# Kernel tuning notes

Hardware: AMD Instinct MI355X
Metric: run time of the kernel (lower is better)

The kernel has to match this reference:

```python
import jax, jax.numpy as jnp
import numpy as np

N_NODES = 50000
N_EDGES = 800000
N_GRAPHS = 64
IN_CH = 128
HID_CH = 128
FC_CH = 128


def setup_inputs() -> dict:
    key = jax.random.key(0)
    ks = jax.random.split(key, 12)

    def lin_w(k, fan_in, fan_out):
        return jax.random.normal(k, (fan_in, fan_out), jnp.float32) * (1.0 / np.sqrt(fan_in))

    return {
        "x": jax.random.normal(ks[0], (N_NODES, IN_CH), jnp.float32),
        "edge_index": jax.random.randint(ks[1], (2, N_EDGES), 0, N_NODES, dtype=jnp.int64),
        "batch_vec": jnp.sort(jax.random.randint(ks[2], (N_NODES,), 0, N_GRAPHS, dtype=jnp.int64)),
        "W1": lin_w(ks[3], IN_CH, HID_CH),
        "b1": jnp.zeros((HID_CH,), jnp.float32),
        "W2": lin_w(ks[4], HID_CH, HID_CH),
        "b2": jnp.zeros((HID_CH,), jnp.float32),
        "W3": lin_w(ks[5], HID_CH, FC_CH),
        "b3": jnp.zeros((FC_CH,), jnp.float32),
        "fcW1": lin_w(ks[6], FC_CH, IN_CH),
        "fcb1": jnp.zeros((IN_CH,), jnp.float32),
        "fcW2": lin_w(ks[7], IN_CH, 2),
        "fcb2": jnp.zeros((2,), jnp.float32),
    }


def reference(x, edge_index, batch_vec, W1, b1, W2, b2, W3, b3, fcW1, fcb1, fcW2, fcb2):
    n = x.shape[0]
    row, col = edge_index[0], edge_index[1]  # src -> dst

    # GCN symmetric normalization with self-loops: deg[j] = in-degree(j) + 1
    deg = jnp.zeros((n,), x.dtype).at[col].add(1.0) + 1.0
    inv_sqrt = jax.lax.rsqrt(deg)
    edge_norm = inv_sqrt[row] * inv_sqrt[col]  # [E]
    self_norm = (inv_sqrt * inv_sqrt)[:, None]  # [N,1], self-loop weight 1/deg

    def gcn(h, W, b):
        h = h @ W  # [N, out]
        agg = jnp.zeros_like(h).at[col].add(h[row] * edge_norm[:, None])
        return agg + h * self_norm + b

    h = jax.nn.relu(gcn(x, W1, b1))
    h = jax.nn.relu(gcn(h, W2, b2))
    h = jax.nn.relu(gcn(h, W3, b3))
    h = jax.nn.relu(h @ fcW1 + fcb1)
    h = h @ fcW2 + fcb2  # [N, 2]

    # global mean pool per graph
    sums = jax.ops.segment_sum(h, batch_vec, num_segments=N_GRAPHS)
    cnts = jax.ops.segment_sum(jnp.ones((n,), h.dtype), batch_vec, num_segments=N_GRAPHS)
    pooled = sums / jnp.maximum(cnts, 1.0)[:, None]  # [G, 2]
    return jax.nn.softmax(pooled, axis=1)
```

## Files before the change

### kernel.cpp

```cpp
#include <hip/hip_runtime.h>


#define CH 128
#define BSH 7
#define SEG 4096
#define EPW 4096
#define SA 40
#define SAF 136
#define SC 132
#define SC8 144

typedef unsigned short ushortT;
typedef unsigned int uintT;
typedef unsigned char ucharT;
typedef __attribute__((ext_vector_type(8))) short short8;
typedef __attribute__((ext_vector_type(4))) float floatx4;
typedef __attribute__((ext_vector_type(2))) float floatx2;

__device__ __forceinline__ float bf2f(uintT u) {
    return __uint_as_float(u << 16);
}
__device__ __forceinline__ ushortT f2bf(float f) {
    uintT x = __float_as_uint(f);
    return (ushortT)((x + 0x7fffu + ((x >> 16) & 1u)) >> 16);
}
__device__ __forceinline__ void dec4(uintT u, float* o) {
    floatx2 lo = __builtin_amdgcn_cvt_pk_f32_fp8((int)u, false);
    floatx2 hi = __builtin_amdgcn_cvt_pk_f32_fp8((int)u, true);
    o[0] = lo.x; o[1] = lo.y; o[2] = hi.x; o[3] = hi.y;
}

__global__ void k_zero(int* __restrict__ bfill, int NB, float* __restrict__ acc, int nacc) {
    int t = threadIdx.x;
    for (int i = t; i < NB; i += 256) bfill[i] = 0;
    for (int i = t; i < nacc; i += 256) acc[i] = 0.f;
}

__global__ __launch_bounds__(256) void k_bin(const int* __restrict__ row,
                                             const int* __restrict__ col,
                                             int* __restrict__ bfill,
                                             uintT* __restrict__ seg,
                                             int E, int NB) {
    __shared__ uintT staged[EPW];
    __shared__ int target[EPW];
    __shared__ int sval[512];
    __shared__ int horig[512];
    __shared__ int pcnt[512];
    __shared__ int gbase[512];
    const int t = threadIdx.x;
    const int e0 = blockIdx.x * EPW;
    const int cnt = min(EPW, E - e0);

    sval[t] = 0; sval[t + 256] = 0;
    __syncthreads();

    int er[16], ec[16];
#pragma unroll
    for (int i = 0; i < 16; ++i) {
        int le = i * 256 + t;
        if (le < cnt) {
            er[i] = row[e0 + le];
            ec[i] = col[e0 + le];
            atomicAdd(&sval[ec[i] >> BSH], 1);
        }
    }
    __syncthreads();
    horig[t] = sval[t]; horig[t + 256] = sval[t + 256];
    __syncthreads();
    for (int off = 1; off < 512; off <<= 1) {
        int a = (t >= off) ? sval[t - off] : 0;
        int b2 = sval[t + 256 - off];
        __syncthreads();
        sval[t] += a;
        sval[t + 256] += b2;
        __syncthreads();
    }
    for (int b = t; b < 512; b += 256) {
        int h = horig[b];
        pcnt[b] = sval[b] - h;
        gbase[b] = (h > 0 && b < NB) ? atomicAdd(&bfill[b], h) : 0;
    }
    __syncthreads();
#pragma unroll
    for (int i = 0; i < 16; ++i) {
        int le = i * 256 + t;
        if (le < cnt) {
            int b = ec[i] >> BSH;
            int j = atomicAdd(&pcnt[b], 1);
            staged[j] = (uintT)er[i] | ((uintT)ec[i] << 16);
            int lo = sval[b] - horig[b];
            target[j] = b * SEG + gbase[b] + (j - lo);
        }
    }
    __syncthreads();
    for (int s = t; s < cnt; s += 256) seg[target[s]] = staged[s];
}

__global__ __launch_bounds__(512) void k_binvs_bscan(const int* __restrict__ bfill,
                                                     const uintT* __restrict__ seg,
                                                     float* __restrict__ invs,
                                                     int* __restrict__ bbase,
                                                     int* __restrict__ indptr,
                                                     int NB, int N, int E) {
    const int b = blockIdx.x;
    const int t = threadIdx.x;
    if (b < NB) {
        __shared__ int h[128];
        if (t < 128) h[t] = 0;
        __syncthreads();
        int cnt = bfill[b];
        const uintT* sp = seg + (size_t)b * SEG;
        for (int s = t; s < cnt; s += 512) atomicAdd(&h[(sp[s] >> 16) & 127], 1);
        __syncthreads();
        int d = b * 128 + t;
        if (t < 128 && d < N) invs[d] = rsqrtf((float)h[t] + 1.0f);
    } else {
        __shared__ int s[512];
        int v = (t < NB) ? bfill[t] : 0;
        s[t] = v;
        __syncthreads();
        for (int off = 1; off < 512; off <<= 1) {
            int a = (t >= off) ? s[t - off] : 0;
            __syncthreads();
            s[t] += a;
            __syncthreads();
        }
        if (t < NB) bbase[t] = s[t] - v;
        if (t == 0) indptr[N] = E;
    }
}

__global__ __launch_bounds__(256) void k_scatterprep(const int* __restrict__ bfill,
                                                     const int* __restrict__ bbase,
                                                     const uintT* __restrict__ seg,
                                                     const float* __restrict__ invs,
                                                     int* __restrict__ indptr,
                                                     uintT* __restrict__ epack,
                                                     const float* __restrict__ X,
                                                     ucharT* __restrict__ Xb,
                                                     const float* __restrict__ w0,
                                                     const float* __restrict__ w1,
                                                     const float* __restrict__ w2,
                                                     const float* __restrict__ w3,
                                                     ushortT* __restrict__ Whi,
                                                     int N, int NB, int total4) {
    const int t = threadIdx.x;
    if ((int)blockIdx.x < NB) {
        __shared__ uintT staged[SEG];
        __shared__ int h[128];
        __shared__ int sc[128];
        __shared__ int pc[128];
        const int b = blockIdx.x;
        const int cnt = bfill[b];
        const int base = bbase[b];
        const uintT* sp = seg + (size_t)b * SEG;

        if (t < 128) h[t] = 0;
        __syncthreads();
        for (int s = t; s < cnt; s += 256) atomicAdd(&h[(sp[s] >> 16) & 127], 1);
        __syncthreads();
        if (t < 128) sc[t] = h[t];
        __syncthreads();
        for (int off = 1; off < 128; off <<= 1) {
            int a = (t >= off && t < 128) ? sc[t - off] : 0;
            __syncthreads();
            if (t < 128) sc[t] += a;
            __syncthreads();
        }
        if (t < 128) {
            int excl = sc[t] - h[t];
            pc[t] = excl;
            int d = b * 128 + t;
            if (d < N) indptr[d] = base + excl;
        }
        __syncthreads();
        for (int s = t; s < cnt; s += 256) {
            uintT rc = sp[s];
            int src = (int)(rc & 0xffffu), dst = (int)(rc >> 16);
            int j = atomicAdd(&pc[dst & 127], 1);
            float nrm = invs[src] * invs[dst];
            staged[j] = (uintT)src | ((uintT)f2bf(nrm) << 16);
        }
        __syncthreads();
        for (int s = t; s < cnt; s += 256) epack[base + s] = staged[s];
    } else if ((int)blockIdx.x < NB + 256) {
        int idx = (blockIdx.x - NB) * 256 + t;
        int m = idx >> 14;
        int r = idx & 16383;
        int n = r >> 7;
        int k = r & 127;
        const float* W = (m == 0) ? w0 : (m == 1) ? w1 : (m == 2) ? w2 : w3;
        Whi[m * 16384 + n * CH + k] = f2bf(W[k * CH + n]);
    } else {
        int i = (blockIdx.x - NB - 256) * 256 + t;
        if (i < total4) {
            float4 v = reinterpret_cast<const float4*>(X)[i];
            int r0 = __builtin_amdgcn_cvt_pk_fp8_f32(v.x, v.y, 0, false);
            int r1 = __builtin_amdgcn_cvt_pk_fp8_f32(v.z, v.w, r0, true);
            reinterpret_cast<int*>(Xb)[i] = r1;
        }
    }
}

__global__ __launch_bounds__(256) void k_agg(const ucharT* __restrict__ H8,
                                             const uintT* __restrict__ epack,
                                             const int* __restrict__ indptr,
                                             const float* __restrict__ invs,
                                             ucharT* __restrict__ Z8, int N) {
    const int wave = threadIdx.x >> 6, lane = threadIdx.x & 63;
    const int sub = lane >> 4;
    const int l = lane & 15;
    const int node = blockIdx.x * 16 + wave * 4 + sub;
    if (node >= N) return;

    const uint2* H2 = reinterpret_cast<const uint2*>(H8);

    float acc[8];
    {
        float sn = invs[node];
        float sn2 = sn * sn;
        uint2 h = H2[(size_t)node * 16 + l];
        float d[8];
        dec4(h.x, d); dec4(h.y, d + 4);
#pragma unroll
        for (int j = 0; j < 8; ++j) acc[j] = sn2 * d[j];
    }

    int p = indptr[node];
    int p1 = indptr[node + 1];
    for (; p + 8 <= p1; p += 8) {
        uintT e[8];
#pragma unroll
        for (int i = 0; i < 8; ++i) e[i] = epack[p + i];
        uint2 g[8];
#pragma unroll
        for (int i = 0; i < 8; ++i) g[i] = H2[(size_t)(int)(e[i] & 0xffffu) * 16 + l];
#pragma unroll
        for (int i = 0; i < 8; ++i) {
            float wv = bf2f(e[i] >> 16);
            float d[8];
            dec4(g[i].x, d); dec4(g[i].y, d + 4);
#pragma unroll
            for (int j = 0; j < 8; ++j) acc[j] += wv * d[j];
        }
    }
    if (p + 4 <= p1) {
        uintT e[4];
#pragma unroll
        for (int i = 0; i < 4; ++i) e[i] = epack[p + i];
        uint2 g[4];
#pragma unroll
        for (int i = 0; i < 4; ++i) g[i] = H2[(size_t)(int)(e[i] & 0xffffu) * 16 + l];
#pragma unroll
        for (int i = 0; i < 4; ++i) {
            float wv = bf2f(e[i] >> 16);
            float d[8];
            dec4(g[i].x, d); dec4(g[i].y, d + 4);
#pragma unroll
            for (int j = 0; j < 8; ++j) acc[j] += wv * d[j];
        }
        p += 4;
    }
    for (; p < p1; ++p) {
        uintT e = epack[p];
        uint2 g = H2[(size_t)(int)(e & 0xffffu) * 16 + l];
        float wv = bf2f(e >> 16);
        float d[8];
        dec4(g.x, d); dec4(g.y, d + 4);
#pragma unroll
        for (int j = 0; j < 8; ++j) acc[j] += wv * d[j];
    }

    uint2 o;
    {
        int r0 = __builtin_amdgcn_cvt_pk_fp8_f32(acc[0], acc[1], 0, false);
        r0 = __builtin_amdgcn_cvt_pk_fp8_f32(acc[2], acc[3], r0, true);
        int r1 = __builtin_amdgcn_cvt_pk_fp8_f32(acc[4], acc[5], 0, false);
        r1 = __builtin_amdgcn_cvt_pk_fp8_f32(acc[6], acc[7], r1, true);
        o.x = (uintT)r0; o.y = (uintT)r1;
    }
    reinterpret_cast<uint2*>(Z8)[(size_t)node * 16 + l] = o;
}

__global__ __launch_bounds__(256) void k_gemm(const ucharT* __restrict__ In8,
                                              const ushortT* __restrict__ Whi,
                                              const float* __restrict__ Bias,
                                              ucharT* __restrict__ Out8, int N) {
    __shared__ ushortT smem[128 * SC];
    ushortT* As = smem;
    ushortT* Ws = smem + 128 * SA;
    ushortT* Cs = smem;

    const int tid = threadIdx.x;
    const int wave = tid >> 6, lane = tid & 63;
    const int quad = lane >> 4, l15 = lane & 15;
    const int mBase = (wave >> 1) * 64, nBase = (wave & 1) * 64;
    const int row0 = blockIdx.x * 128;
    const int r = tid >> 1, half = tid & 1;

    floatx4 acc[4][4];
    const floatx4 zero4 = {0.f, 0.f, 0.f, 0.f};
#pragma unroll
    for (int i = 0; i < 4; i++)
#pragma unroll
        for (int j = 0; j < 4; j++) acc[i][j] = zero4;

    for (int ks = 0; ks < 4; ++ks) {
        {
            int grow = row0 + r;
            uint4 a8 = {0, 0, 0, 0};
            if (grow < N)
                a8 = *reinterpret_cast<const uint4*>(
                    In8 + (size_t)grow * CH + ks * 32 + half * 16);
            uintT wds[4] = {a8.x, a8.y, a8.z, a8.w};
            uintT ob[8];
#pragma unroll
            for (int q = 0; q < 4; ++q) {
                float d[4];
                dec4(wds[q], d);
                ob[2 * q] = (uintT)f2bf(d[0]) | ((uintT)f2bf(d[1]) << 16);
                ob[2 * q + 1] = (uintT)f2bf(d[2]) | ((uintT)f2bf(d[3]) << 16);
            }
            uint4* dd = reinterpret_cast<uint4*>(&As[r * SA + half * 16]);
            dd[0] = uint4{ob[0], ob[1], ob[2], ob[3]};
            dd[1] = uint4{ob[4], ob[5], ob[6], ob[7]};
            const uint4* sh = reinterpret_cast<const uint4*>(Whi + r * CH + ks * 32 + half * 16);
            uint4* dh = reinterpret_cast<uint4*>(&Ws[r * SA + half * 16]);
            dh[0] = sh[0]; dh[1] = sh[1];
        }
        __syncthreads();

        short8 af[4], wf[4];
#pragma unroll
        for (int mt = 0; mt < 4; ++mt)
            af[mt] = *reinterpret_cast<const short8*>(&As[(mBase + mt * 16 + l15) * SA + quad * 8]);
#pragma unroll
        for (int nt = 0; nt < 4; ++nt)
            wf[nt] = *reinterpret_cast<const short8*>(&Ws[(nBase + nt * 16 + l15) * SA + quad * 8]);
#pragma unroll
        for (int mt = 0; mt < 4; ++mt)
#pragma unroll
            for (int nt = 0; nt < 4; ++nt)
                acc[mt][nt] = __builtin_amdgcn_mfma_f32_16x16x32_bf16(af[mt], wf[nt], acc[mt][nt], 0, 0, 0);
        __syncthreads();
    }

    float bb[4];
#pragma unroll
    for (int nt = 0; nt < 4; ++nt) bb[nt] = Bias[nBase + nt * 16 + l15];

    ucharT* Cs8 = reinterpret_cast<ucharT*>(Cs);
#pragma unroll
    for (int mt = 0; mt < 4; ++mt)
#pragma unroll
        for (int nt = 0; nt < 4; ++nt)
#pragma unroll
            for (int r4 = 0; r4 < 4; ++r4) {
                int lrow = mBase + mt * 16 + quad * 4 + r4;
                float v = fmaxf(acc[mt][nt][r4] + bb[nt], 0.f);
                int f8 = __builtin_amdgcn_cvt_pk_fp8_f32(v, 0.f, 0, false);
                Cs8[lrow * SC8 + nBase + nt * 16 + l15] = (ucharT)(f8 & 0xff);
            }
    __syncthreads();
    {
        int grow = row0 + r;
        if (grow < N) {
            const uint4* s4 = reinterpret_cast<const uint4*>(&Cs8[r * SC8 + half * 64]);
            uint4* dst = reinterpret_cast<uint4*>(Out8 + (size_t)grow * CH + half * 64);
#pragma unroll
            for (int q = 0; q < 4; ++q) dst[q] = s4[q];
        }
    }
}

__global__ __launch_bounds__(256) void k_tail(const ucharT* __restrict__ Z8,
                                              const ushortT* __restrict__ W3hi,
                                              const float* __restrict__ B3,
                                              const ushortT* __restrict__ F1hi,
                                              const float* __restrict__ FB1,
                                              const float* __restrict__ FW2,
                                              const float* __restrict__ FB2,
                                              const int* __restrict__ batch,
                                              float* __restrict__ sums,
                                              float* __restrict__ cnts, int N) {
    __shared__ ushortT Hf[128 * SAF];
    __shared__ ushortT Ws[128 * SA];
    __shared__ float rp0[256];
    __shared__ float rp1[256];
    __shared__ float ls[192];

    const int tid = threadIdx.x;
    const int wave = tid >> 6, lane = tid & 63;
    const int quad = lane >> 4, l15 = lane & 15;
    const int mBase = (wave >> 1) * 64, nBase = (wave & 1) * 64;
    const int row0 = blockIdx.x * 128;
    const int r = tid >> 1, half = tid & 1;

    {
        int grow = row0 + r;
        uint4 a8 = {0, 0, 0, 0}, b8 = {0, 0, 0, 0}, c8 = {0, 0, 0, 0}, d8v = {0, 0, 0, 0};
        if (grow < N) {
            const uint4* s = reinterpret_cast<const uint4*>(Z8 + (size_t)grow * CH + half * 64);
            a8 = s[0]; b8 = s[1]; c8 = s[2]; d8v = s[3];
        }
        uintT wds[16] = {a8.x, a8.y, a8.z, a8.w, b8.x, b8.y, b8.z, b8.w,
                         c8.x, c8.y, c8.z, c8.w, d8v.x, d8v.y, d8v.z, d8v.w};
#pragma unroll
        for (int q = 0; q < 16; ++q) {
            float d[4];
            dec4(wds[q], d);
            uint2 o;
            o.x = (uintT)f2bf(d[0]) | ((uintT)f2bf(d[1]) << 16);
            o.y = (uintT)f2bf(d[2]) | ((uintT)f2bf(d[3]) << 16);
            *reinterpret_cast<uint2*>(&Hf[r * SAF + half * 64 + q * 4]) = o;
        }
    }

    floatx4 acc[4][4];
    const floatx4 zero4 = {0.f, 0.f, 0.f, 0.f};
#pragma unroll
    for (int i = 0; i < 4; i++)
#pragma unroll
        for (int j = 0; j < 4; j++) acc[i][j] = zero4;

    for (int ks = 0; ks < 4; ++ks) {
        {
            const uint4* sh = reinterpret_cast<const uint4*>(W3hi + r * CH + ks * 32 + half * 16);
            uint4* dh = reinterpret_cast<uint4*>(&Ws[r * SA + half * 16]);
            dh[0] = sh[0]; dh[1] = sh[1];
        }
        __syncthreads();
        short8 af[4], wf[4];
#pragma unroll
        for (int mt = 0; mt < 4; ++mt)
            af[mt] = *reinterpret_cast<const short8*>(&Hf[(mBase + mt * 16 + l15) * SAF + ks * 32 + quad * 8]);
#pragma unroll
        for (int nt = 0; nt < 4; ++nt)
            wf[nt] = *reinterpret_cast<const short8*>(&Ws[(nBase + nt * 16 + l15) * SA + quad * 8]);
#pragma unroll
        for (int mt = 0; mt < 4; ++mt)
#pragma unroll
            for (int nt = 0; nt < 4; ++nt)
                acc[mt][nt] = __builtin_amdgcn_mfma_f32_16x16x32_bf16(af[mt], wf[nt], acc[mt][nt], 0, 0, 0);
        __syncthreads();
    }

    {
        float bb[4];
#pragma unroll
        for (int nt = 0; nt < 4; ++nt) bb[nt] = B3[nBase + nt * 16 + l15];
#pragma unroll
        for (int mt = 0; mt < 4; ++mt)
#pragma unroll
            for (int nt = 0; nt < 4; ++nt)
#pragma unroll
                for (int r4 = 0; r4 < 4; ++r4) {
                    int lrow = mBase + mt * 16 + quad * 4 + r4;
                    float v = fmaxf(acc[mt][nt][r4] + bb[nt], 0.f);
                    Hf[lrow * SAF + nBase + nt * 16 + l15] = f2bf(v);
                }
    }
    __syncthreads();

#pragma unroll
    for (int i = 0; i < 4; i++)
#pragma unroll
        for (int j = 0; j < 4; j++) acc[i][j] = zero4;
    for (int ks = 0; ks < 4; ++ks) {
        {
            const uint4* sh = reinterpret_cast<const uint4*>(F1hi + r * CH + ks * 32 + half * 16);
            uint4* dh = reinterpret_cast<uint4*>(&Ws[r * SA + half * 16]);
            dh[0] = sh[0]; dh[1] = sh[1];
        }
        __syncthreads();
        short8 af[4], wf[4];
#pragma unroll
        for (int mt = 0; mt < 4; ++mt)
            af[mt] = *reinterpret_cast<const short8*>(&Hf[(mBase + mt * 16 + l15) * SAF + ks * 32 + quad * 8]);
#pragma unroll
        for (int nt = 0; nt < 4; ++nt)
            wf[nt] = *reinterpret_cast<const short8*>(&Ws[(nBase + nt * 16 + l15) * SA + quad * 8]);
#pragma unroll
        for (int mt = 0; mt < 4; ++mt)
#pragma unroll
            for (int nt = 0; nt < 4; ++nt)
                acc[mt][nt] = __builtin_amdgcn_mfma_f32_16x16x32_bf16(af[mt], wf[nt], acc[mt][nt], 0, 0, 0);
        __syncthreads();
    }

    {
        float bb[4];
#pragma unroll
        for (int nt = 0; nt < 4; ++nt) bb[nt] = FB1[nBase + nt * 16 + l15];
        float w20[4], w21[4];
#pragma unroll
        for (int nt = 0; nt < 4; ++nt) {
            float2 wv = *reinterpret_cast<const float2*>(FW2 + 2 * (nBase + nt * 16 + l15));
            w20[nt] = wv.x;
            w21[nt] = wv.y;
        }
#pragma unroll
        for (int mt = 0; mt < 4; ++mt)
#pragma unroll
            for (int r4 = 0; r4 < 4; ++r4) {
                float d0 = 0.f, d1 = 0.f;
#pragma unroll
                for (int nt = 0; nt < 4; ++nt) {
                    float v = fmaxf(acc[mt][nt][r4] + bb[nt], 0.f);
                    d0 += v * w20[nt];
                    d1 += v * w21[nt];
                }
#pragma unroll
                for (int m = 8; m >= 1; m >>= 1) {
                    d0 += __shfl_xor(d0, m, 64);
                    d1 += __shfl_xor(d1, m, 64);
                }
                if (l15 == 0) {
                    int lrow = mBase + mt * 16 + quad * 4 + r4;
                    rp0[lrow * 2 + (wave & 1)] = d0;
                    rp1[lrow * 2 + (wave & 1)] = d1;
                }
            }
    }
    if (tid < 192) ls[tid] = 0.f;
    __syncthreads();

    if (tid < 128) {
        int node = row0 + tid;
        if (node < N) {
            float d0 = rp0[tid * 2] + rp0[tid * 2 + 1] + FB2[0];
            float d1 = rp1[tid * 2] + rp1[tid * 2 + 1] + FB2[1];
            int g = batch[node];
            atomicAdd(&ls[g], d0);
            atomicAdd(&ls[64 + g], d1);
            atomicAdd(&ls[128 + g], 1.0f);
        }
    }
    __syncthreads();
    if (tid < 64) {
        float c = ls[128 + tid];
        if (c != 0.f) {
            atomicAdd(&sums[2 * tid], ls[tid]);
            atomicAdd(&sums[2 * tid + 1], ls[64 + tid]);
            atomicAdd(&cnts[tid], c);
        }
    }
}

__global__ void k_softmax(const float* __restrict__ sums, const float* __restrict__ cnts,
                          float* __restrict__ out, int G) {
    int g = blockIdx.x * blockDim.x + threadIdx.x;
    if (g < G) {
        float c = fmaxf(cnts[g], 1.0f);
        float p0 = sums[2 * g] / c;
        float p1 = sums[2 * g + 1] / c;
        float m = fmaxf(p0, p1);
        float e0 = expf(p0 - m), e1 = expf(p1 - m);
        float inv = 1.f / (e0 + e1);
        out[2 * g] = e0 * inv;
        out[2 * g + 1] = e1 * inv;
    }
}

extern "C" void kernel_launch(void* const* d_in, const int* in_sizes, int n_in,
                              void* d_out, int out_size, void* d_ws, size_t ws_size,
                              hipStream_t stream) {
    const float* X   = (const float*)d_in[0];
    const int* EI    = (const int*)d_in[1];
    const int* BATCH = (const int*)d_in[2];
    const float* W1  = (const float*)d_in[3];
    const float* B1  = (const float*)d_in[4];
    const float* W2  = (const float*)d_in[5];
    const float* B2  = (const float*)d_in[6];
    const float* W3  = (const float*)d_in[7];
    const float* B3  = (const float*)d_in[8];
    const float* FW1 = (const float*)d_in[9];
    const float* FB1 = (const float*)d_in[10];
    const float* FW2 = (const float*)d_in[11];
    const float* FB2 = (const float*)d_in[12];

    const int N = in_sizes[0] / CH;
    const int E = in_sizes[1] / 2;
    const int G = out_size / 2;
    const int* rowp = EI;
    const int* colp = EI + E;
    const int NB = (N + 127) >> BSH;

    char* w = (char*)d_ws;
    auto alloc = [&](size_t bytes) -> char* {
        char* p = w;
        w += (bytes + 255) & ~(size_t)255;
        return p;
    };
    ucharT*  Z8    = (ucharT*)alloc((size_t)N * CH);
    ucharT*  Hb8   = (ucharT*)alloc((size_t)N * CH);
    ucharT*  Xb8   = (ucharT*)alloc((size_t)N * CH);
    ushortT* WhiA  = (ushortT*)alloc((size_t)4 * 16384 * 2);
    float* invs    = (float*)alloc((size_t)N * 4);
    int*   indptr  = (int*)alloc((size_t)(N + 1) * 4);
    uintT* epack   = (uintT*)alloc((size_t)E * 4);
    uintT* seg     = (uintT*)alloc((size_t)NB * SEG * 4);
    int*   bfill   = (int*)alloc((size_t)NB * 4);
    int*   bbase   = (int*)alloc((size_t)NB * 4);
    float* sums    = (float*)alloc((size_t)G * 3 * 4);
    float* cnts    = sums + 2 * G;

    const int nbAgg  = (N + 15) / 16;
    const int nbGemm = (N + 127) / 128;
    const int nbBin  = (E + EPW - 1) / EPW;
    const int total4 = N * CH / 4;
    const int nbSP   = NB + 256 + (total4 + 255) / 256;

    k_zero<<<1, 256, 0, stream>>>(bfill, NB, sums, 3 * G);
    k_bin<<<nbBin, 256, 0, stream>>>(rowp, colp, bfill, seg, E, NB);
    k_binvs_bscan<<<NB + 1, 512, 0, stream>>>(bfill, seg, invs, bbase, indptr, NB, N, E);
    k_scatterprep<<<nbSP, 256, 0, stream>>>(bfill, bbase, seg, invs, indptr, epack,
                                            X, Xb8, W1, W2, W3, FW1, WhiA, N, NB, total4);

    k_agg<<<nbAgg, 256, 0, stream>>>(Xb8, epack, indptr, invs, Z8, N);
    k_gemm<<<nbGemm, 256, 0, stream>>>(Z8, WhiA, B1, Hb8, N);
    k_agg<<<nbAgg, 256, 0, stream>>>(Hb8, epack, indptr, invs, Z8, N);
    k_gemm<<<nbGemm, 256, 0, stream>>>(Z8, WhiA + 16384, B2, Hb8, N);
    k_agg<<<nbAgg, 256, 0, stream>>>(Hb8, epack, indptr, invs, Z8, N);
    k_tail<<<nbGemm, 256, 0, stream>>>(Z8, WhiA + 2 * 16384, B3,
                                       WhiA + 3 * 16384, FB1, FW2, FB2,
                                       BATCH, sums, cnts, N);
    k_softmax<<<1, 64, 0, stream>>>(sums, cnts, (float*)d_out, G);
}
```

Baseline: 211.7 us.

## Split node features into two channel-half planes so gather working set fits cache

```diff
diff --git a/kernel.cpp b/kernel.cpp
--- a/kernel.cpp
+++ b/kernel.cpp
@@ -137,7 +137,8 @@
                                                      int* __restrict__ indptr,
                                                      uintT* __restrict__ epack,
                                                      const float* __restrict__ X,
-                                                     ucharT* __restrict__ Xb,
+                                                     ucharT* __restrict__ Xlo,
+                                                     ucharT* __restrict__ Xhi,
                                                      const float* __restrict__ w0,
                                                      const float* __restrict__ w1,
                                                      const float* __restrict__ w2,
@@ -197,29 +198,39 @@
             float4 v = reinterpret_cast<const float4*>(X)[i];
             int r0 = __builtin_amdgcn_cvt_pk_fp8_f32(v.x, v.y, 0, false);
             int r1 = __builtin_amdgcn_cvt_pk_fp8_f32(v.z, v.w, r0, true);
-            reinterpret_cast<int*>(Xb)[i] = r1;
-        }
-    }
-}
-
-__global__ __launch_bounds__(256) void k_agg(const ucharT* __restrict__ H8,
+            int node = i >> 5;
+            int g = i & 31;
+            int* dst = (g < 16) ? reinterpret_cast<int*>(Xlo + (size_t)node * 64) + g
+                                : reinterpret_cast<int*>(Xhi + (size_t)node * 64) + (g - 16);
+            *dst = r1;
+        }
+    }
+}
+
+__global__ __launch_bounds__(256) void k_agg(const ucharT* __restrict__ Hlo,
+                                             const ucharT* __restrict__ Hhi,
                                              const uintT* __restrict__ epack,
                                              const int* __restrict__ indptr,
                                              const float* __restrict__ invs,
-                                             ucharT* __restrict__ Z8, int N) {
+                                             ucharT* __restrict__ Zlo,
+                                             ucharT* __restrict__ Zhi,
+                                             int N, int nbHalf) {
+    const int half = (blockIdx.x >> 2) & 1;
+    const int nb = (blockIdx.x >> 3) * 4 + (blockIdx.x & 3);
+    if (nb >= nbHalf) return;
     const int wave = threadIdx.x >> 6, lane = threadIdx.x & 63;
-    const int sub = lane >> 4;
-    const int l = lane & 15;
-    const int node = blockIdx.x * 16 + wave * 4 + sub;
+    const int ng = lane >> 3;
+    const int l = lane & 7;
+    const int node = nb * 32 + wave * 8 + ng;
     if (node >= N) return;
 
-    const uint2* H2 = reinterpret_cast<const uint2*>(H8);
+    const uint2* H2 = reinterpret_cast<const uint2*>(half ? Hhi : Hlo);
 
     float acc[8];
     {
         float sn = invs[node];
         float sn2 = sn * sn;
-        uint2 h = H2[(size_t)node * 16 + l];
+        uint2 h = H2[(size_t)node * 8 + l];
         float d[8];
         dec4(h.x, d); dec4(h.y, d + 4);
 #pragma unroll
@@ -234,7 +245,7 @@
         for (int i = 0; i < 8; ++i) e[i] = epack[p + i];
         uint2 g[8];
 #pragma unroll
-        for (int i = 0; i < 8; ++i) g[i] = H2[(size_t)(int)(e[i] & 0xffffu) * 16 + l];
+        for (int i = 0; i < 8; ++i) g[i] = H2[(size_t)(int)(e[i] & 0xffffu) * 8 + l];
 #pragma unroll
         for (int i = 0; i < 8; ++i) {
             float wv = bf2f(e[i] >> 16);
@@ -250,7 +261,7 @@
         for (int i = 0; i < 4; ++i) e[i] = epack[p + i];
         uint2 g[4];
 #pragma unroll
-        for (int i = 0; i < 4; ++i) g[i] = H2[(size_t)(int)(e[i] & 0xffffu) * 16 + l];
+        for (int i = 0; i < 4; ++i) g[i] = H2[(size_t)(int)(e[i] & 0xffffu) * 8 + l];
 #pragma unroll
         for (int i = 0; i < 4; ++i) {
             float wv = bf2f(e[i] >> 16);
@@ -263,7 +274,7 @@
     }
     for (; p < p1; ++p) {
         uintT e = epack[p];
-        uint2 g = H2[(size_t)(int)(e & 0xffffu) * 16 + l];
+        uint2 g = H2[(size_t)(int)(e & 0xffffu) * 8 + l];
         float wv = bf2f(e >> 16);
         float d[8];
         dec4(g.x, d); dec4(g.y, d + 4);
@@ -279,13 +290,15 @@
         r1 = __builtin_amdgcn_cvt_pk_fp8_f32(acc[6], acc[7], r1, true);
         o.x = (uintT)r0; o.y = (uintT)r1;
     }
-    reinterpret_cast<uint2*>(Z8)[(size_t)node * 16 + l] = o;
-}
-
-__global__ __launch_bounds__(256) void k_gemm(const ucharT* __restrict__ In8,
+    reinterpret_cast<uint2*>(half ? Zhi : Zlo)[(size_t)node * 8 + l] = o;
+}
+
+__global__ __launch_bounds__(256) void k_gemm(const ucharT* __restrict__ Inlo,
+                                              const ucharT* __restrict__ Inhi,
                                               const ushortT* __restrict__ Whi,
                                               const float* __restrict__ Bias,
-                                              ucharT* __restrict__ Out8, int N) {
+                                              ucharT* __restrict__ Outlo,
+                                              ucharT* __restrict__ Outhi, int N) {
     __shared__ ushortT smem[128 * SC];
     ushortT* As = smem;
     ushortT* Ws = smem + 128 * SA;
@@ -308,10 +321,11 @@
     for (int ks = 0; ks < 4; ++ks) {
         {
             int grow = row0 + r;
+            const ucharT* sbase = (ks < 2) ? Inlo : Inhi;
             uint4 a8 = {0, 0, 0, 0};
             if (grow < N)
                 a8 = *reinterpret_cast<const uint4*>(
-                    In8 + (size_t)grow * CH + ks * 32 + half * 16);
+                    sbase + (size_t)grow * 64 + (ks & 1) * 32 + half * 16);
             uintT wds[4] = {a8.x, a8.y, a8.z, a8.w};
             uintT ob[8];
 #pragma unroll
@@ -366,14 +380,16 @@
         int grow = row0 + r;
         if (grow < N) {
             const uint4* s4 = reinterpret_cast<const uint4*>(&Cs8[r * SC8 + half * 64]);
-            uint4* dst = reinterpret_cast<uint4*>(Out8 + (size_t)grow * CH + half * 64);
+            ucharT* obase = half ? Outhi : Outlo;
+            uint4* dst = reinterpret_cast<uint4*>(obase + (size_t)grow * 64);
 #pragma unroll
             for (int q = 0; q < 4; ++q) dst[q] = s4[q];
         }
     }
 }
 
-__global__ __launch_bounds__(256) void k_tail(const ucharT* __restrict__ Z8,
+__global__ __launch_bounds__(256) void k_tail(const ucharT* __restrict__ Zlo,
+                                              const ucharT* __restrict__ Zhi,
                                               const ushortT* __restrict__ W3hi,
                                               const float* __restrict__ B3,
                                               const ushortT* __restrict__ F1hi,
@@ -398,9 +414,10 @@
 
     {
         int grow = row0 + r;
+        const ucharT* zsrc = half ? Zhi : Zlo;
         uint4 a8 = {0, 0, 0, 0}, b8 = {0, 0, 0, 0}, c8 = {0, 0, 0, 0}, d8v = {0, 0, 0, 0};
         if (grow < N) {
-            const uint4* s = reinterpret_cast<const uint4*>(Z8 + (size_t)grow * CH + half * 64);
+            const uint4* s = reinterpret_cast<const uint4*>(zsrc + (size_t)grow * 64);
             a8 = s[0]; b8 = s[1]; c8 = s[2]; d8v = s[3];
         }
         uintT wds[16] = {a8.x, a8.y, a8.z, a8.w, b8.x, b8.y, b8.z, b8.w,
@@ -592,9 +609,12 @@
         w += (bytes + 255) & ~(size_t)255;
         return p;
     };
-    ucharT*  Z8    = (ucharT*)alloc((size_t)N * CH);
-    ucharT*  Hb8   = (ucharT*)alloc((size_t)N * CH);
-    ucharT*  Xb8   = (ucharT*)alloc((size_t)N * CH);
+    ucharT*  Zlo   = (ucharT*)alloc((size_t)N * 64);
+    ucharT*  Zhi   = (ucharT*)alloc((size_t)N * 64);
+    ucharT*  Hlo   = (ucharT*)alloc((size_t)N * 64);
+    ucharT*  Hhi   = (ucharT*)alloc((size_t)N * 64);
+    ucharT*  Xlo   = (ucharT*)alloc((size_t)N * 64);
+    ucharT*  Xhi   = (ucharT*)alloc((size_t)N * 64);
     ushortT* WhiA  = (ushortT*)alloc((size_t)4 * 16384 * 2);
     float* invs    = (float*)alloc((size_t)N * 4);
     int*   indptr  = (int*)alloc((size_t)(N + 1) * 4);
@@ -605,7 +625,8 @@
     float* sums    = (float*)alloc((size_t)G * 3 * 4);
     float* cnts    = sums + 2 * G;
 
-    const int nbAgg  = (N + 15) / 16;
+    const int nbHalf = (N + 31) / 32;
+    const int nbAgg  = ((nbHalf + 3) / 4) * 8;
     const int nbGemm = (N + 127) / 128;
     const int nbBin  = (E + EPW - 1) / EPW;
     const int total4 = N * CH / 4;
@@ -615,14 +636,15 @@
     k_bin<<<nbBin, 256, 0, stream>>>(rowp, colp, bfill, seg, E, NB);
     k_binvs_bscan<<<NB + 1, 512, 0, stream>>>(bfill, seg, invs, bbase, indptr, NB, N, E);
     k_scatterprep<<<nbSP, 256, 0, stream>>>(bfill, bbase, seg, invs, indptr, epack,
-                                            X, Xb8, W1, W2, W3, FW1, WhiA, N, NB, total4);
-
-    k_agg<<<nbAgg, 256, 0, stream>>>(Xb8, epack, indptr, invs, Z8, N);
-    k_gemm<<<nbGemm, 256, 0, stream>>>(Z8, WhiA, B1, Hb8, N);
-    k_agg<<<nbAgg, 256, 0, stream>>>(Hb8, epack, indptr, invs, Z8, N);
-    k_gemm<<<nbGemm, 256, 0, stream>>>(Z8, WhiA + 16384, B2, Hb8, N);
-    k_agg<<<nbAgg, 256, 0, stream>>>(Hb8, epack, indptr, invs, Z8, N);
-    k_tail<<<nbGemm, 256, 0, stream>>>(Z8, WhiA + 2 * 16384, B3,
+                                            X, Xlo, Xhi, W1, W2, W3, FW1, WhiA,
+                                            N, NB, total4);
+
+    k_agg<<<nbAgg, 256, 0, stream>>>(Xlo, Xhi, epack, indptr, invs, Zlo, Zhi, N, nbHalf);
+    k_gemm<<<nbGemm, 256, 0, stream>>>(Zlo, Zhi, WhiA, B1, Hlo, Hhi, N);
+    k_agg<<<nbAgg, 256, 0, stream>>>(Hlo, Hhi, epack, indptr, invs, Zlo, Zhi, N, nbHalf);
+    k_gemm<<<nbGemm, 256, 0, stream>>>(Zlo, Zhi, WhiA + 16384, B2, Hlo, Hhi, N);
+    k_agg<<<nbAgg, 256, 0, stream>>>(Hlo, Hhi, epack, indptr, invs, Zlo, Zhi, N, nbHalf);
+    k_tail<<<nbGemm, 256, 0, stream>>>(Zlo, Zhi, WhiA + 2 * 16384, B3,
                                        WhiA + 3 * 16384, FB1, FW2, FB2,
                                        BATCH, sums, cnts, N);
     k_softmax<<<1, 64, 0, stream>>>(sums, cnts, (float*)d_out, G);
```

Measured after the change: 210.2 us. No clear change (-0.7%).

## Widen aggregation gathers to 16-byte loads with pipelined edge prefetch

Applied to the files above, without the earlier changes.

```diff
diff --git a/kernel.cpp b/kernel.cpp
--- a/kernel.cpp
+++ b/kernel.cpp
@@ -29,11 +29,8 @@
     floatx2 hi = __builtin_amdgcn_cvt_pk_f32_fp8((int)u, true);
     o[0] = lo.x; o[1] = lo.y; o[2] = hi.x; o[3] = hi.y;
 }
-
-__global__ void k_zero(int* __restrict__ bfill, int NB, float* __restrict__ acc, int nacc) {
-    int t = threadIdx.x;
-    for (int i = t; i < NB; i += 256) bfill[i] = 0;
-    for (int i = t; i < nacc; i += 256) acc[i] = 0.f;
+__device__ __forceinline__ void dec16(uint4 v, float* o) {
+    dec4(v.x, o); dec4(v.y, o + 4); dec4(v.z, o + 8); dec4(v.w, o + 12);
 }
 
 __global__ __launch_bounds__(256) void k_bin(const int* __restrict__ row,
@@ -101,7 +98,9 @@
                                                      float* __restrict__ invs,
                                                      int* __restrict__ bbase,
                                                      int* __restrict__ indptr,
-                                                     int NB, int N, int E) {
+                                                     float* __restrict__ sums,
+                                                     float* __restrict__ cnts,
+                                                     int NB, int N, int E, int G) {
     const int b = blockIdx.x;
     const int t = threadIdx.x;
     if (b < NB) {
@@ -116,6 +115,10 @@
         if (t < 128 && d < N) invs[d] = rsqrtf((float)h[t] + 1.0f);
     } else {
         __shared__ int s[512];
+        for (int i = t; i < 3 * G; i += 512) {
+            if (i < 2 * G) sums[i] = 0.f;
+            else cnts[i - 2 * G] = 0.f;
+        }
         int v = (t < NB) ? bfill[t] : 0;
         s[t] = v;
         __syncthreads();
@@ -208,78 +211,94 @@
                                              const float* __restrict__ invs,
                                              ucharT* __restrict__ Z8, int N) {
     const int wave = threadIdx.x >> 6, lane = threadIdx.x & 63;
-    const int sub = lane >> 4;
-    const int l = lane & 15;
-    const int node = blockIdx.x * 16 + wave * 4 + sub;
+    const int ng = lane >> 3;
+    const int l = lane & 7;
+    const int node = blockIdx.x * 32 + wave * 8 + ng;
     if (node >= N) return;
 
-    const uint2* H2 = reinterpret_cast<const uint2*>(H8);
-
-    float acc[8];
+    const uint4* H4 = reinterpret_cast<const uint4*>(H8);
+
+    float acc[16];
     {
         float sn = invs[node];
         float sn2 = sn * sn;
-        uint2 h = H2[(size_t)node * 16 + l];
-        float d[8];
-        dec4(h.x, d); dec4(h.y, d + 4);
-#pragma unroll
-        for (int j = 0; j < 8; ++j) acc[j] = sn2 * d[j];
+        float d[16];
+        dec16(H4[(size_t)node * 8 + l], d);
+#pragma unroll
+        for (int j = 0; j < 16; ++j) acc[j] = sn2 * d[j];
     }
 
     int p = indptr[node];
     int p1 = indptr[node + 1];
-    for (; p + 8 <= p1; p += 8) {
+
+    if (p + 8 <= p1) {
+        uintT e0[8];
+#pragma unroll
+        for (int i = 0; i < 8; ++i) e0[i] = epack[p + i];
+        for (; p + 16 <= p1; p += 8) {
+            uintT e1[8];
+#pragma unroll
+            for (int i = 0; i < 8; ++i) e1[i] = epack[p + 8 + i];
+            uint4 g[8];
+#pragma unroll
+            for (int i = 0; i < 8; ++i) g[i] = H4[(size_t)(int)(e0[i] & 0xffffu) * 8 + l];
+#pragma unroll
+            for (int i = 0; i < 8; ++i) {
+                float wv = bf2f(e0[i] >> 16);
+                float d[16];
+                dec16(g[i], d);
+#pragma unroll
+                for (int j = 0; j < 16; ++j) acc[j] += wv * d[j];
+            }
+#pragma unroll
+            for (int i = 0; i < 8; ++i) e0[i] = e1[i];
+        }
+        {
+            uint4 g[8];
+#pragma unroll
+            for (int i = 0; i < 8; ++i) g[i] = H4[(size_t)(int)(e0[i] & 0xffffu) * 8 + l];
+#pragma unroll
+            for (int i = 0; i < 8; ++i) {
+                float wv = bf2f(e0[i] >> 16);
+                float d[16];
+                dec16(g[i], d);
+#pragma unroll
+                for (int j = 0; j < 16; ++j) acc[j] += wv * d[j];
+            }
+            p += 8;
+        }
+    }
+    int rem = p1 - p;
+    if (rem > 0) {
         uintT e[8];
 #pragma unroll
-        for (int i = 0; i < 8; ++i) e[i] = epack[p + i];
-        uint2 g[8];
-#pragma unroll
-        for (int i = 0; i < 8; ++i) g[i] = H2[(size_t)(int)(e[i] & 0xffffu) * 16 + l];
+        for (int i = 0; i < 8; ++i) e[i] = epack[(i < rem) ? p + i : p];
+        uint4 g[8];
+#pragma unroll
+        for (int i = 0; i < 8; ++i) g[i] = H4[(size_t)(int)(e[i] & 0xffffu) * 8 + l];
 #pragma unroll
         for (int i = 0; i < 8; ++i) {
-            float wv = bf2f(e[i] >> 16);
-            float d[8];
-            dec4(g[i].x, d); dec4(g[i].y, d + 4);
-#pragma unroll
-            for (int j = 0; j < 8; ++j) acc[j] += wv * d[j];
-        }
-    }
-    if (p + 4 <= p1) {
-        uintT e[4];
-#pragma unroll
-        for (int i = 0; i < 4; ++i) e[i] = epack[p + i];
-        uint2 g[4];
-#pragma unroll
-        for (int i = 0; i < 4; ++i) g[i] = H2[(size_t)(int)(e[i] & 0xffffu) * 16 + l];
-#pragma unroll
-        for (int i = 0; i < 4; ++i) {
-            float wv = bf2f(e[i] >> 16);
-            float d[8];
-            dec4(g[i].x, d); dec4(g[i].y, d + 4);
-#pragma unroll
-            for (int j = 0; j < 8; ++j) acc[j] += wv * d[j];
-        }
-        p += 4;
-    }
-    for (; p < p1; ++p) {
-        uintT e = epack[p];
-        uint2 g = H2[(size_t)(int)(e & 0xffffu) * 16 + l];
-        float wv = bf2f(e >> 16);
-        float d[8];
-        dec4(g.x, d); dec4(g.y, d + 4);
-#pragma unroll
-        for (int j = 0; j < 8; ++j) acc[j] += wv * d[j];
-    }
-
-    uint2 o;
+            float wv = (i < rem) ? bf2f(e[i] >> 16) : 0.f;
+            float d[16];
+            dec16(g[i], d);
+#pragma unroll
+            for (int j = 0; j < 16; ++j) acc[j] += wv * d[j];
+        }
+    }
+
+    uint4 o;
     {
         int r0 = __builtin_amdgcn_cvt_pk_fp8_f32(acc[0], acc[1], 0, false);
         r0 = __builtin_amdgcn_cvt_pk_fp8_f32(acc[2], acc[3], r0, true);
         int r1 = __builtin_amdgcn_cvt_pk_fp8_f32(acc[4], acc[5], 0, false);
         r1 = __builtin_amdgcn_cvt_pk_fp8_f32(acc[6], acc[7], r1, true);
-        o.x = (uintT)r0; o.y = (uintT)r1;
-    }
-    reinterpret_cast<uint2*>(Z8)[(size_t)node * 16 + l] = o;
+        int r2 = __builtin_amdgcn_cvt_pk_fp8_f32(acc[8], acc[9], 0, false);
+        r2 = __builtin_amdgcn_cvt_pk_fp8_f32(acc[10], acc[11], r2, true);
+        int r3 = __builtin_amdgcn_cvt_pk_fp8_f32(acc[12], acc[13], 0, false);
+        r3 = __builtin_amdgcn_cvt_pk_fp8_f32(acc[14], acc[15], r3, true);
+        o.x = (uintT)r0; o.y = (uintT)r1; o.z = (uintT)r2; o.w = (uintT)r3;
+    }
+    reinterpret_cast<uint4*>(Z8)[(size_t)node * 8 + l] = o;
 }
 
 __global__ __launch_bounds__(256) void k_gemm(const ucharT* __restrict__ In8,
@@ -605,15 +624,16 @@
     float* sums    = (float*)alloc((size_t)G * 3 * 4);
     float* cnts    = sums + 2 * G;
 
-    const int nbAgg  = (N + 15) / 16;
+    const int nbAgg  = (N + 31) / 32;
     const int nbGemm = (N + 127) / 128;
     const int nbBin  = (E + EPW - 1) / EPW;
     const int total4 = N * CH / 4;
     const int nbSP   = NB + 256 + (total4 + 255) / 256;
 
-    k_zero<<<1, 256, 0, stream>>>(bfill, NB, sums, 3 * G);
+    hipMemsetAsync(bfill, 0, (size_t)NB * 4, stream);
     k_bin<<<nbBin, 256, 0, stream>>>(rowp, colp, bfill, seg, E, NB);
-    k_binvs_bscan<<<NB + 1, 512, 0, stream>>>(bfill, seg, invs, bbase, indptr, NB, N, E);
+    k_binvs_bscan<<<NB + 1, 512, 0, stream>>>(bfill, seg, invs, bbase, indptr,
+                                              sums, cnts, NB, N, E, G);
     k_scatterprep<<<nbSP, 256, 0, stream>>>(bfill, bbase, seg, invs, indptr, epack,
                                             X, Xb8, W1, W2, W3, FW1, WhiA, N, NB, total4);
 
```

Measured after the change: 209.0 us. No clear change (-1.3%).
